# Performance work log

Hardware: AMD Instinct MI355X
Metric: run time of the kernel (lower is better)

## Reference

```python
import jax, jax.numpy as jnp
import numpy as np

EPS = 1e-6

def _normalize(A):
    # zero the diagonal, add self-loops
    n = A.shape[-1]
    eye = jnp.eye(n, dtype=A.dtype)
    A_hat = A * (1.0 - eye) + eye  # [B,N,N]
    # symmetric degree normalization with eps inside as in the TF code:
    # d = 1/(eps + sqrt(rowsum)); norm = diag(d) @ A_hat @ diag(d)
    d = 1.0 / (EPS + jnp.sqrt(jnp.sum(A_hat, axis=2)))  # [B,N]
    return A_hat * d[:, :, None] * d[:, None, :]


def setup_inputs() -> dict:
    key = jax.random.key(0)
    k1, k2, k3 = jax.random.split(key, 3)
    B, N, F, O = 8, 2048, 128, 128
    x = jax.random.normal(k1, (B, N, F), dtype=jnp.float32)
    adj = jax.random.uniform(k2, (B, N, N), dtype=jnp.float32)
    kernel = jax.random.normal(k3, (F, O), dtype=jnp.float32) * 0.05
    return {"x": x, "adj": adj, "kernel": kernel}


def reference(x, adj, kernel):
    norm = _normalize(adj)                      # [B,N,N]
    agg = jnp.einsum('bnm,bmf->bnf', norm, x)   # batch_dot
    out = jnp.einsum('bnf,fo->bno', agg, kernel)
    return jax.nn.relu(out)
```

## Files before the change

kernel.cpp:

```cpp
#include <hip/hip_runtime.h>


typedef __bf16 bf16x8 __attribute__((ext_vector_type(8)));
typedef __bf16 bf16x4 __attribute__((ext_vector_type(4)));
typedef float  f32x4  __attribute__((ext_vector_type(4)));

#define NN 2048
#define NB 8

__device__ __forceinline__ void load_lds16(__bf16* lds, const __bf16* g) {
    __builtin_amdgcn_global_load_lds(
        (const __attribute__((address_space(1))) void*)g,
        (__attribute__((address_space(3))) void*)lds, 16, 0, 0);
}

__global__ __launch_bounds__(256) void d_kernel(const float* __restrict__ adj,
                                                float* __restrict__ dvec,
                                                const float* __restrict__ W,
                                                __bf16* __restrict__ Wt) {
    if (blockIdx.x >= NB * NN / 4) {
        int idx = (blockIdx.x - NB * NN / 4) * 256 + threadIdx.x;
        int f = idx >> 7, o = idx & 127;
        Wt[o * 128 + f] = (__bf16)W[idx];
        return;
    }
    const int lane = threadIdx.x & 63;
    const int row  = blockIdx.x * 4 + (threadIdx.x >> 6);
    const float* rp = adj + (size_t)row * NN;
    float4 s4 = {0.f, 0.f, 0.f, 0.f};
#pragma unroll
    for (int it = 0; it < 8; ++it) {
        float4 v = *(const float4*)(rp + it * 256 + lane * 4);
        s4.x += v.x; s4.y += v.y; s4.z += v.z; s4.w += v.w;
    }
    float s = (s4.x + s4.y) + (s4.z + s4.w);
#pragma unroll
    for (int off = 32; off; off >>= 1) s += __shfl_down(s, off);
    if (lane == 0) {
        int n = row & (NN - 1);
        float sh = s - rp[n] + 1.0f;
        dvec[row] = 1.0f / (1e-6f + sqrtf(sh));
    }
}

__global__ __launch_bounds__(256) void xw_kernel(const float* __restrict__ x,
                                                 const __bf16* __restrict__ Wt,
                                                 const float* __restrict__ dvec,
                                                 __bf16* __restrict__ yt) {
    const int lane = threadIdx.x & 63;
    const int wave = threadIdx.x >> 6;
    const int b    = blockIdx.x & 7;
    const int mt   = (blockIdx.x >> 3) * 4 + wave;
    const int m0   = mt * 16;
    const int kgrp = (lane >> 4) * 8;
    const float* xp = x + ((size_t)b * NN + m0 + (lane & 15)) * 128 + kgrp;

    f32x4 acc[8];
#pragma unroll
    for (int i = 0; i < 8; ++i) acc[i] = (f32x4){0.f, 0.f, 0.f, 0.f};

#pragma unroll
    for (int kt = 0; kt < 4; ++kt) {
        f32x4 a0 = *(const f32x4*)(xp + kt * 32);
        f32x4 a1 = *(const f32x4*)(xp + kt * 32 + 4);
        float av[8] = {a0.x, a0.y, a0.z, a0.w, a1.x, a1.y, a1.z, a1.w};
        bf16x8 af;
#pragma unroll
        for (int j = 0; j < 8; ++j) af[j] = (__bf16)av[j];
#pragma unroll
        for (int nb = 0; nb < 8; ++nb) {
            bf16x8 bfv = *(const bf16x8*)(Wt + (nb * 16 + (lane & 15)) * 128 +
                                          kt * 32 + kgrp);
            acc[nb] = __builtin_amdgcn_mfma_f32_16x16x32_bf16(af, bfv, acc[nb], 0, 0, 0);
        }
    }
    const int col0 = lane & 15;
    const int rq   = (lane >> 4) * 4;
#pragma unroll
    for (int r = 0; r < 4; ++r) {
        int m = m0 + rq + r;
        float dm = dvec[b * NN + m];
#pragma unroll
        for (int nb = 0; nb < 8; ++nb) {
            int o = nb * 16 + col0;
            yt[((size_t)b * 128 + o) * NN + m] = (__bf16)(acc[nb][r] * dm);
        }
    }
}

__global__ __launch_bounds__(256) void gemm_kernel(const float* __restrict__ adj,
                                                   const __bf16* __restrict__ yt,
                                                   const float* __restrict__ dvec,
                                                   float* __restrict__ out) {
    __shared__ alignas(16) __bf16 sB[2][128][32];

    const int tid  = threadIdx.x;
    const int wave = tid >> 6;
    const int lane = tid & 63;
    const int b    = blockIdx.x & 7;
    const int tile = blockIdx.x >> 3;
    const int rsel = (wave & 1) * 16;
    const int csel = (wave >> 1) * 64;
    const int kgrp = (lane >> 4) * 8;

    const int arow_loc = tile * 32 + rsel + (lane & 15);
    const float* ap = adj + ((size_t)b * NN + arow_loc) * NN + kgrp;

    const __bf16* ytb = yt + (size_t)b * 128 * NN;
    const int b_row0 = wave * 32;
    const __bf16* b_src = ytb + (size_t)(b_row0 + (lane >> 2)) * NN + (lane & 3) * 8;

    f32x4 acc[4];
#pragma unroll
    for (int i = 0; i < 4; ++i) acc[i] = (f32x4){0.f, 0.f, 0.f, 0.f};

    load_lds16(&sB[0][b_row0][0], b_src);
    load_lds16(&sB[0][b_row0 + 16][0], b_src + (size_t)16 * NN);
    f32x4 ca0 = *(const f32x4*)(ap);
    f32x4 ca1 = *(const f32x4*)(ap + 4);

    for (int kt = 0; kt < 64; ++kt) {
        const int cur = kt & 1;
        __syncthreads();

        f32x4 na0, na1;
        if (kt + 1 < 64) {
            const __bf16* bs = b_src + (size_t)(kt + 1) * 32;
            load_lds16(&sB[cur ^ 1][b_row0][0], bs);
            load_lds16(&sB[cur ^ 1][b_row0 + 16][0], bs + (size_t)16 * NN);
            na0 = *(const f32x4*)(ap + (kt + 1) * 32);
            na1 = *(const f32x4*)(ap + (kt + 1) * 32 + 4);
        }

        bf16x8 af;
        af[0] = (__bf16)ca0.x; af[1] = (__bf16)ca0.y;
        af[2] = (__bf16)ca0.z; af[3] = (__bf16)ca0.w;
        af[4] = (__bf16)ca1.x; af[5] = (__bf16)ca1.y;
        af[6] = (__bf16)ca1.z; af[7] = (__bf16)ca1.w;

#pragma unroll
        for (int nb = 0; nb < 4; ++nb) {
            bf16x8 bfv = *(const bf16x8*)(
                &sB[cur][csel + nb * 16 + (lane & 15)][kgrp]);
            acc[nb] = __builtin_amdgcn_mfma_f32_16x16x32_bf16(af, bfv, acc[nb], 0, 0, 0);
        }
        ca0 = na0; ca1 = na1;
    }

    const int col0 = lane & 15;
    const int rq   = (lane >> 4) * 4;
#pragma unroll
    for (int r = 0; r < 4; ++r) {
        int n_loc = tile * 32 + rsel + rq + r;
        size_t grow = (size_t)b * NN + n_loc;
        float dn   = dvec[grow];
        float cfac = 1.0f - adj[grow * NN + n_loc];
#pragma unroll
        for (int nb = 0; nb < 4; ++nb) {
            int o = csel + nb * 16 + col0;
            float yp = (float)ytb[(size_t)o * NN + n_loc];
            float v = (acc[nb][r] + cfac * yp) * dn;
            out[grow * 128 + o] = v > 0.f ? v : 0.f;
        }
    }
}

extern "C" void kernel_launch(void* const* d_in, const int* in_sizes, int n_in,
                              void* d_out, int out_size, void* d_ws, size_t ws_size,
                              hipStream_t stream) {
    const float* x   = (const float*)d_in[0];
    const float* adj = (const float*)d_in[1];
    const float* W   = (const float*)d_in[2];
    float* out = (float*)d_out;

    char* ws = (char*)d_ws;
    float*  dvec = (float*)ws;
    __bf16* Wt   = (__bf16*)(ws + (64 << 10));
    __bf16* yt   = (__bf16*)(ws + (128 << 10));

    hipLaunchKernelGGL(d_kernel, dim3(NB * NN / 4 + 64), dim3(256), 0, stream,
                       adj, dvec, W, Wt);
    hipLaunchKernelGGL(xw_kernel, dim3(256), dim3(256), 0, stream, x, Wt, dvec, yt);
    hipLaunchKernelGGL(gemm_kernel, dim3(512), dim3(256), 0, stream,
                       adj, yt, dvec, out);
}
```

Measured before the change: 244.2 us.

## Fuse degree, weight transpose and XW kernels into one pre-pass kernel

Merges the degree-vector reduction, the W transpose and the X·W product into a single kernel. The W transpose now goes into swizzled LDS in each block rather than global memory. The column-side degree scaling moves from the XW output into the main GEMM's A-operand conversion, which removes the dependency of XW on dvec and one launch. In exchange the GEMM does extra dvec loads and multiplies in its inner loop, and row-sum work is split unevenly across blocks.

```diff
diff --git a/kernel.cpp b/kernel.cpp
--- a/kernel.cpp
+++ b/kernel.cpp
@@ -2,7 +2,6 @@
 
 
 typedef __bf16 bf16x8 __attribute__((ext_vector_type(8)));
-typedef __bf16 bf16x4 __attribute__((ext_vector_type(4)));
 typedef float  f32x4  __attribute__((ext_vector_type(4)));
 
 #define NN 2048
@@ -14,43 +13,62 @@
         (__attribute__((address_space(3))) void*)lds, 16, 0, 0);
 }
 
-__global__ __launch_bounds__(256) void d_kernel(const float* __restrict__ adj,
-                                                float* __restrict__ dvec,
-                                                const float* __restrict__ W,
-                                                __bf16* __restrict__ Wt) {
-    if (blockIdx.x >= NB * NN / 4) {
-        int idx = (blockIdx.x - NB * NN / 4) * 256 + threadIdx.x;
-        int f = idx >> 7, o = idx & 127;
-        Wt[o * 128 + f] = (__bf16)W[idx];
-        return;
-    }
-    const int lane = threadIdx.x & 63;
-    const int row  = blockIdx.x * 4 + (threadIdx.x >> 6);
-    const float* rp = adj + (size_t)row * NN;
-    float4 s4 = {0.f, 0.f, 0.f, 0.f};
-#pragma unroll
-    for (int it = 0; it < 8; ++it) {
-        float4 v = *(const float4*)(rp + it * 256 + lane * 4);
-        s4.x += v.x; s4.y += v.y; s4.z += v.z; s4.w += v.w;
-    }
-    float s = (s4.x + s4.y) + (s4.z + s4.w);
-#pragma unroll
-    for (int off = 32; off; off >>= 1) s += __shfl_down(s, off);
-    if (lane == 0) {
-        int n = row & (NN - 1);
-        float sh = s - rp[n] + 1.0f;
-        dvec[row] = 1.0f / (1e-6f + sqrtf(sh));
-    }
-}
-
-__global__ __launch_bounds__(256) void xw_kernel(const float* __restrict__ x,
-                                                 const __bf16* __restrict__ Wt,
-                                                 const float* __restrict__ dvec,
-                                                 __bf16* __restrict__ yt) {
+__global__ __launch_bounds__(256) void pre_kernel(const float* __restrict__ x,
+                                                  const float* __restrict__ adj,
+                                                  const float* __restrict__ W,
+                                                  float* __restrict__ dvec,
+                                                  __bf16* __restrict__ yt) {
+    __shared__ __bf16 WtL[128 * 128];
+
+    const int bid  = blockIdx.x;
     const int lane = threadIdx.x & 63;
     const int wave = threadIdx.x >> 6;
-    const int b    = blockIdx.x & 7;
-    const int mt   = (blockIdx.x >> 3) * 4 + wave;
+
+    int rbase, rcnt;
+    if (bid < 256) { rbase = bid * 24;                rcnt = 6;  }
+    else           { rbase = 6144 + (bid - 256) * 40; rcnt = 10; }
+
+    for (int i = 0; i < rcnt; ++i) {
+        const int row = rbase + wave * rcnt + i;
+        const float* rp = adj + (size_t)row * NN;
+        float4 s4 = {0.f, 0.f, 0.f, 0.f};
+#pragma unroll
+        for (int it = 0; it < 8; ++it) {
+            float4 v = *(const float4*)(rp + it * 256 + lane * 4);
+            s4.x += v.x; s4.y += v.y; s4.z += v.z; s4.w += v.w;
+        }
+        float s = (s4.x + s4.y) + (s4.z + s4.w);
+#pragma unroll
+        for (int off = 32; off; off >>= 1) s += __shfl_down(s, off);
+        if (lane == 0) {
+            int n = row & (NN - 1);
+            float sh = s - rp[n] + 1.0f;
+            dvec[row] = 1.0f / (1e-6f + sqrtf(sh));
+        }
+    }
+
+    if (bid >= 256) return;
+
+    {
+        const int t  = threadIdx.x;
+        const int f  = t >> 1;
+        const int o0 = (t & 1) * 64;
+        const float* wp = W + f * 128 + o0;
+#pragma unroll
+        for (int j = 0; j < 64; j += 4) {
+            float4 w4 = *(const float4*)(wp + j);
+            float wv[4] = {w4.x, w4.y, w4.z, w4.w};
+#pragma unroll
+            for (int u = 0; u < 4; ++u) {
+                int o = o0 + j + u;
+                WtL[o * 128 + (f ^ ((o & 7) << 3))] = (__bf16)wv[u];
+            }
+        }
+    }
+    __syncthreads();
+
+    const int b    = bid & 7;
+    const int mt   = (bid >> 3) * 4 + wave;
     const int m0   = mt * 16;
     const int kgrp = (lane >> 4) * 8;
     const float* xp = x + ((size_t)b * NN + m0 + (lane & 15)) * 128 + kgrp;
@@ -69,8 +87,9 @@
         for (int j = 0; j < 8; ++j) af[j] = (__bf16)av[j];
 #pragma unroll
         for (int nb = 0; nb < 8; ++nb) {
-            bf16x8 bfv = *(const bf16x8*)(Wt + (nb * 16 + (lane & 15)) * 128 +
-                                          kt * 32 + kgrp);
+            int c = nb * 16 + (lane & 15);
+            bf16x8 bfv = *(const bf16x8*)(
+                &WtL[c * 128 + ((kt * 32 + kgrp) ^ ((c & 7) << 3))]);
             acc[nb] = __builtin_amdgcn_mfma_f32_16x16x32_bf16(af, bfv, acc[nb], 0, 0, 0);
         }
     }
@@ -79,11 +98,10 @@
 #pragma unroll
     for (int r = 0; r < 4; ++r) {
         int m = m0 + rq + r;
-        float dm = dvec[b * NN + m];
 #pragma unroll
         for (int nb = 0; nb < 8; ++nb) {
             int o = nb * 16 + col0;
-            yt[((size_t)b * 128 + o) * NN + m] = (__bf16)(acc[nb][r] * dm);
+            yt[((size_t)b * 128 + o) * NN + m] = (__bf16)acc[nb][r];
         }
     }
 }
@@ -105,6 +123,7 @@
 
     const int arow_loc = tile * 32 + rsel + (lane & 15);
     const float* ap = adj + ((size_t)b * NN + arow_loc) * NN + kgrp;
+    const float* dp = dvec + b * NN + kgrp;
 
     const __bf16* ytb = yt + (size_t)b * 128 * NN;
     const int b_row0 = wave * 32;
@@ -118,25 +137,29 @@
     load_lds16(&sB[0][b_row0 + 16][0], b_src + (size_t)16 * NN);
     f32x4 ca0 = *(const f32x4*)(ap);
     f32x4 ca1 = *(const f32x4*)(ap + 4);
+    f32x4 cd0 = *(const f32x4*)(dp);
+    f32x4 cd1 = *(const f32x4*)(dp + 4);
 
     for (int kt = 0; kt < 64; ++kt) {
         const int cur = kt & 1;
         __syncthreads();
 
-        f32x4 na0, na1;
+        f32x4 na0, na1, nd0, nd1;
         if (kt + 1 < 64) {
             const __bf16* bs = b_src + (size_t)(kt + 1) * 32;
             load_lds16(&sB[cur ^ 1][b_row0][0], bs);
             load_lds16(&sB[cur ^ 1][b_row0 + 16][0], bs + (size_t)16 * NN);
             na0 = *(const f32x4*)(ap + (kt + 1) * 32);
             na1 = *(const f32x4*)(ap + (kt + 1) * 32 + 4);
+            nd0 = *(const f32x4*)(dp + (kt + 1) * 32);
+            nd1 = *(const f32x4*)(dp + (kt + 1) * 32 + 4);
         }
 
         bf16x8 af;
-        af[0] = (__bf16)ca0.x; af[1] = (__bf16)ca0.y;
-        af[2] = (__bf16)ca0.z; af[3] = (__bf16)ca0.w;
-        af[4] = (__bf16)ca1.x; af[5] = (__bf16)ca1.y;
-        af[6] = (__bf16)ca1.z; af[7] = (__bf16)ca1.w;
+        af[0] = (__bf16)(ca0.x * cd0.x); af[1] = (__bf16)(ca0.y * cd0.y);
+        af[2] = (__bf16)(ca0.z * cd0.z); af[3] = (__bf16)(ca0.w * cd0.w);
+        af[4] = (__bf16)(ca1.x * cd1.x); af[5] = (__bf16)(ca1.y * cd1.y);
+        af[6] = (__bf16)(ca1.z * cd1.z); af[7] = (__bf16)(ca1.w * cd1.w);
 
 #pragma unroll
         for (int nb = 0; nb < 4; ++nb) {
@@ -144,7 +167,7 @@
                 &sB[cur][csel + nb * 16 + (lane & 15)][kgrp]);
             acc[nb] = __builtin_amdgcn_mfma_f32_16x16x32_bf16(af, bfv, acc[nb], 0, 0, 0);
         }
-        ca0 = na0; ca1 = na1;
+        ca0 = na0; ca1 = na1; cd0 = nd0; cd1 = nd1;
     }
 
     const int col0 = lane & 15;
@@ -154,7 +177,7 @@
         int n_loc = tile * 32 + rsel + rq + r;
         size_t grow = (size_t)b * NN + n_loc;
         float dn   = dvec[grow];
-        float cfac = 1.0f - adj[grow * NN + n_loc];
+        float cfac = (1.0f - adj[grow * NN + n_loc]) * dn;
 #pragma unroll
         for (int nb = 0; nb < 4; ++nb) {
             int o = csel + nb * 16 + col0;
@@ -175,12 +198,10 @@
 
     char* ws = (char*)d_ws;
     float*  dvec = (float*)ws;
-    __bf16* Wt   = (__bf16*)(ws + (64 << 10));
     __bf16* yt   = (__bf16*)(ws + (128 << 10));
 
-    hipLaunchKernelGGL(d_kernel, dim3(NB * NN / 4 + 64), dim3(256), 0, stream,
-                       adj, dvec, W, Wt);
-    hipLaunchKernelGGL(xw_kernel, dim3(256), dim3(256), 0, stream, x, Wt, dvec, yt);
+    hipLaunchKernelGGL(pre_kernel, dim3(512), dim3(256), 0, stream,
+                       x, adj, W, dvec, yt);
     hipLaunchKernelGGL(gemm_kernel, dim3(512), dim3(256), 0, stream,
                        adj, yt, dvec, out);
 }
```

Result: slower. 251.2 us (+2.9%).

## Drop LDS staging in adj GEMM, shrink tiles, move column scaling into A

Applied to the files above, without the earlier changes.

The aggregation GEMM no longer stages yt through double-buffered shared memory with barriers. Each wave now reads its B fragments straight from global memory and the row tile shrinks from 32 to 16, which doubles the grid to 1024 blocks. The right-hand degree scaling moves out of xw_kernel and is applied to adj elements (multiplied by dvec) before the bf16 conversion, with the self-loop correction rescaled to match. This removes the barrier and LDS cost and adds parallelism, but adj rows are re-read by twice as many blocks, there is extra dvec traffic, and B reuse now depends on the cache.

```diff
diff --git a/kernel.cpp b/kernel.cpp
--- a/kernel.cpp
+++ b/kernel.cpp
@@ -2,17 +2,10 @@
 
 
 typedef __bf16 bf16x8 __attribute__((ext_vector_type(8)));
-typedef __bf16 bf16x4 __attribute__((ext_vector_type(4)));
 typedef float  f32x4  __attribute__((ext_vector_type(4)));
 
 #define NN 2048
 #define NB 8
-
-__device__ __forceinline__ void load_lds16(__bf16* lds, const __bf16* g) {
-    __builtin_amdgcn_global_load_lds(
-        (const __attribute__((address_space(1))) void*)g,
-        (__attribute__((address_space(3))) void*)lds, 16, 0, 0);
-}
 
 __global__ __launch_bounds__(256) void d_kernel(const float* __restrict__ adj,
                                                 float* __restrict__ dvec,
@@ -45,7 +38,6 @@
 
 __global__ __launch_bounds__(256) void xw_kernel(const float* __restrict__ x,
                                                  const __bf16* __restrict__ Wt,
-                                                 const float* __restrict__ dvec,
                                                  __bf16* __restrict__ yt) {
     const int lane = threadIdx.x & 63;
     const int wave = threadIdx.x >> 6;
@@ -79,11 +71,10 @@
 #pragma unroll
     for (int r = 0; r < 4; ++r) {
         int m = m0 + rq + r;
-        float dm = dvec[b * NN + m];
 #pragma unroll
         for (int nb = 0; nb < 8; ++nb) {
             int o = nb * 16 + col0;
-            yt[((size_t)b * 128 + o) * NN + m] = (__bf16)(acc[nb][r] * dm);
+            yt[((size_t)b * 128 + o) * NN + m] = (__bf16)acc[nb][r];
         }
     }
 }
@@ -92,71 +83,56 @@
                                                    const __bf16* __restrict__ yt,
                                                    const float* __restrict__ dvec,
                                                    float* __restrict__ out) {
-    __shared__ alignas(16) __bf16 sB[2][128][32];
-
     const int tid  = threadIdx.x;
     const int wave = tid >> 6;
     const int lane = tid & 63;
     const int b    = blockIdx.x & 7;
     const int tile = blockIdx.x >> 3;
-    const int rsel = (wave & 1) * 16;
-    const int csel = (wave >> 1) * 64;
+    const int csel = wave * 32;
     const int kgrp = (lane >> 4) * 8;
 
-    const int arow_loc = tile * 32 + rsel + (lane & 15);
+    const int arow_loc = tile * 16 + (lane & 15);
     const float* ap = adj + ((size_t)b * NN + arow_loc) * NN + kgrp;
+    const float* dp = dvec + b * NN + kgrp;
 
     const __bf16* ytb = yt + (size_t)b * 128 * NN;
-    const int b_row0 = wave * 32;
-    const __bf16* b_src = ytb + (size_t)(b_row0 + (lane >> 2)) * NN + (lane & 3) * 8;
+    const __bf16* bp  = ytb + (size_t)(csel + (lane & 15)) * NN + kgrp;
 
-    f32x4 acc[4];
+    f32x4 acc[2];
 #pragma unroll
-    for (int i = 0; i < 4; ++i) acc[i] = (f32x4){0.f, 0.f, 0.f, 0.f};
+    for (int i = 0; i < 2; ++i) acc[i] = (f32x4){0.f, 0.f, 0.f, 0.f};
 
-    load_lds16(&sB[0][b_row0][0], b_src);
-    load_lds16(&sB[0][b_row0 + 16][0], b_src + (size_t)16 * NN);
-    f32x4 ca0 = *(const f32x4*)(ap);
-    f32x4 ca1 = *(const f32x4*)(ap + 4);
-
+#pragma unroll 4
     for (int kt = 0; kt < 64; ++kt) {
-        const int cur = kt & 1;
-        __syncthreads();
-
-        f32x4 na0, na1;
-        if (kt + 1 < 64) {
-            const __bf16* bs = b_src + (size_t)(kt + 1) * 32;
-            load_lds16(&sB[cur ^ 1][b_row0][0], bs);
-            load_lds16(&sB[cur ^ 1][b_row0 + 16][0], bs + (size_t)16 * NN);
-            na0 = *(const f32x4*)(ap + (kt + 1) * 32);
-            na1 = *(const f32x4*)(ap + (kt + 1) * 32 + 4);
-        }
+        const int ko = kt * 32;
+        f32x4 a0 = *(const f32x4*)(ap + ko);
+        f32x4 a1 = *(const f32x4*)(ap + ko + 4);
+        f32x4 d0 = *(const f32x4*)(dp + ko);
+        f32x4 d1 = *(const f32x4*)(dp + ko + 4);
 
         bf16x8 af;
-        af[0] = (__bf16)ca0.x; af[1] = (__bf16)ca0.y;
-        af[2] = (__bf16)ca0.z; af[3] = (__bf16)ca0.w;
-        af[4] = (__bf16)ca1.x; af[5] = (__bf16)ca1.y;
-        af[6] = (__bf16)ca1.z; af[7] = (__bf16)ca1.w;
+        af[0] = (__bf16)(a0.x * d0.x); af[1] = (__bf16)(a0.y * d0.y);
+        af[2] = (__bf16)(a0.z * d0.z); af[3] = (__bf16)(a0.w * d0.w);
+        af[4] = (__bf16)(a1.x * d1.x); af[5] = (__bf16)(a1.y * d1.y);
+        af[6] = (__bf16)(a1.z * d1.z); af[7] = (__bf16)(a1.w * d1.w);
 
 #pragma unroll
-        for (int nb = 0; nb < 4; ++nb) {
-            bf16x8 bfv = *(const bf16x8*)(
-                &sB[cur][csel + nb * 16 + (lane & 15)][kgrp]);
+        for (int nb = 0; nb < 2; ++nb) {
+            bf16x8 bfv = *(const bf16x8*)(bp + (size_t)(nb * 16) * NN + ko);
             acc[nb] = __builtin_amdgcn_mfma_f32_16x16x32_bf16(af, bfv, acc[nb], 0, 0, 0);
         }
-        ca0 = na0; ca1 = na1;
     }
 
     const int col0 = lane & 15;
     const int rq   = (lane >> 4) * 4;
 #pragma unroll
     for (int r = 0; r < 4; ++r) {
-        int n_loc = tile * 32 + rsel + rq + r;
+        int n_loc = tile * 16 + rq + r;
         size_t grow = (size_t)b * NN + n_loc;
         float dn   = dvec[grow];
-        float cfac = 1.0f - adj[grow * NN + n_loc];
+        float cfac = (1.0f - adj[grow * NN + n_loc]) * dn;
 #pragma unroll
-        for (int nb = 0; nb < 4; ++nb) {
+        for (int nb = 0; nb < 2; ++nb) {
             int o = csel + nb * 16 + col0;
             float yp = (float)ytb[(size_t)o * NN + n_loc];
             float v = (acc[nb][r] + cfac * yp) * dn;
@@ -180,7 +156,7 @@
 
     hipLaunchKernelGGL(d_kernel, dim3(NB * NN / 4 + 64), dim3(256), 0, stream,
                        adj, dvec, W, Wt);
-    hipLaunchKernelGGL(xw_kernel, dim3(256), dim3(256), 0, stream, x, Wt, dvec, yt);
-    hipLaunchKernelGGL(gemm_kernel, dim3(512), dim3(256), 0, stream,
+    hipLaunchKernelGGL(xw_kernel, dim3(256), dim3(256), 0, stream, x, Wt, yt);
+    hipLaunchKernelGGL(gemm_kernel, dim3(1024), dim3(256), 0, stream,
                        adj, yt, dvec, out);
 }
```

After: 330.6 us. 35.4% more time.
